# Performance work log

Hardware: AMD Instinct MI355X
Metric: run time of the kernel (lower is better)

The kernel has to match this reference:

```python
import jax, jax.numpy as jnp
import numpy as np

D_MODEL = 512
N_HEADS = 8
HEAD_DIM = D_MODEL // N_HEADS
TRUST_BIAS_SCALE = 0.1


def setup_inputs() -> dict:
    key = jax.random.key(0)
    ks = jax.random.split(key, 12)
    B, S, D, HD = 4, 2048, D_MODEL, HEAD_DIM
    s = 1.0 / np.sqrt(D)
    inp = {
        "x": jax.random.normal(ks[0], (B, S, D), dtype=jnp.float32),
        "trust_scores": jax.random.uniform(ks[1], (B, S), dtype=jnp.float32),
        # Linear weights stored as [in, out] (y = x @ W + b), matching torch math.
        "Wq": jax.random.normal(ks[2], (D, D), dtype=jnp.float32) * s,
        "bq": jnp.zeros((D,), dtype=jnp.float32),
        "Wk": jax.random.normal(ks[3], (D, D), dtype=jnp.float32) * s,
        "bk": jnp.zeros((D,), dtype=jnp.float32),
        "Wv": jax.random.normal(ks[4], (D, D), dtype=jnp.float32) * s,
        "bv": jnp.zeros((D,), dtype=jnp.float32),
        # trust_projection: nn.Linear(1, head_dim) -> weight vector [HD]
        "Wt": jax.random.normal(ks[5], (HD,), dtype=jnp.float32),
        "bt": jnp.zeros((HD,), dtype=jnp.float32),
        # trust_gate: nn.Linear(d_model + 1, d_model)
        "Wg": jax.random.normal(ks[6], (D + 1, D), dtype=jnp.float32) * s,
        "bg": jnp.zeros((D,), dtype=jnp.float32),
        "Wo": jax.random.normal(ks[7], (D, D), dtype=jnp.float32) * s,
        "bo": jnp.zeros((D,), dtype=jnp.float32),
    }
    return inp


def reference(x, trust_scores, Wq, bq, Wk, bk, Wv, bv, Wt, bt, Wg, bg, Wo, bo):
    B, S, D = x.shape
    H, HD = N_HEADS, HEAD_DIM

    # q/k/v projections -> [B, H, S, HD]
    q = (x @ Wq + bq).reshape(B, S, H, HD).transpose(0, 2, 1, 3)
    k = (x @ Wk + bk).reshape(B, S, H, HD).transpose(0, 2, 1, 3)
    v = (x @ Wv + bv).reshape(B, S, H, HD).transpose(0, 2, 1, 3)

    scores = jnp.einsum("bhqd,bhkd->bhqk", q, k) / jnp.sqrt(jnp.float32(HD))

    # trust bias: project scalar trust per turn into head_dim, outer-product affinity
    trust_proj = trust_scores[..., None] * Wt + bt            # [B, S, HD]
    trust_affinity = jax.nn.sigmoid(
        jnp.einsum("bqd,bkd->bqk", trust_proj, trust_proj))   # [B, S, S]
    scores = scores + TRUST_BIAS_SCALE * trust_affinity[:, None]  # broadcast heads

    attn = jax.nn.softmax(scores, axis=-1)                    # dropout is identity (eval)
    attended = jnp.einsum("bhqk,bhkd->bqhd", attn, v).reshape(B, S, D)

    # trust gating before output projection
    gate_in = jnp.concatenate([attended, trust_scores[..., None]], axis=-1)
    gate = jax.nn.sigmoid(gate_in @ Wg + bg)
    out = (attended * gate) @ Wo + bo
    return out, attn
```

## Files before the change

### kernel.cpp

```cpp
#include <hip/hip_runtime.h>
#include <math.h>

#define SEQ 2048
#define DM 512
#define NHH 8
#define NB 4
#define MR (NB*SEQ)
#define NBH (NB*NHH)

typedef __attribute__((ext_vector_type(8))) short bf16x8;
typedef __attribute__((ext_vector_type(4))) float f32x4;
#define MFMA __builtin_amdgcn_mfma_f32_16x16x32_bf16

#define OFF_XB   0ull
#define OFF_QB   8388608ull
#define OFF_KB   16777216ull
#define OFF_VB   25165824ull
#define OFF_ATTF 33554432ull
#define OFF_WQT  50331648ull
#define OFF_WKT  50855936ull
#define OFF_WVT  51380224ull
#define OFF_WGT  51904512ull
#define OFF_WOT  52428800ull
#define OFF_TS   52953088ull
#define OUT_ATTN 4194304ull

__device__ __forceinline__ unsigned short f2b(float f) {
  union { float f; unsigned u; } v; v.f = f;
  unsigned r = v.u + 0x7FFFu + ((v.u >> 16) & 1u);
  return (unsigned short)(r >> 16);
}
__device__ __forceinline__ float b2f(unsigned v16) {
  union { unsigned u; float f; } v; v.u = v16 << 16; return v.f;
}
__device__ __forceinline__ float sigm(float x) { return 1.0f / (1.0f + __expf(-x)); }

__global__ void k_trust_scalars(const float* __restrict__ Wt,
                                const float* __restrict__ bt,
                                float* __restrict__ ts) {
  int l = threadIdx.x;
  float w = Wt[l], b = bt[l];
  float a = w * w, bb = w * b, c = b * b;
  #pragma unroll
  for (int off = 32; off; off >>= 1) {
    a  += __shfl_down(a, off);
    bb += __shfl_down(bb, off);
    c  += __shfl_down(c, off);
  }
  if (l == 0) { ts[0] = a; ts[1] = bb; ts[2] = c; }
}

__global__ __launch_bounds__(256) void k_cvt_x(const float* __restrict__ x,
                                               unsigned short* __restrict__ xb) {
  const int i = (blockIdx.x * 256 + threadIdx.x) * 8;
  float4 a = *(const float4*)(x + i);
  float4 b = *(const float4*)(x + i + 4);
  uint4 o;
  o.x = (unsigned)f2b(a.x) | ((unsigned)f2b(a.y) << 16);
  o.y = (unsigned)f2b(a.z) | ((unsigned)f2b(a.w) << 16);
  o.z = (unsigned)f2b(b.x) | ((unsigned)f2b(b.y) << 16);
  o.w = (unsigned)f2b(b.z) | ((unsigned)f2b(b.w) << 16);
  *(uint4*)(xb + i) = o;
}

__global__ __launch_bounds__(256) void k_wtrans(const float* __restrict__ W,
                                                unsigned short* __restrict__ Wt) {
  __shared__ unsigned short tile[64][74];
  const int k0 = blockIdx.x * 64, n0 = blockIdx.y * 64, t = threadIdx.x;
  const int rr = t >> 4, c4 = (t & 15) * 4;
  #pragma unroll
  for (int rep = 0; rep < 4; rep++) {
    const int r = rr + rep * 16;
    float4 v = *(const float4*)(W + (size_t)(k0 + r) * 512 + n0 + c4);
    tile[c4][r] = f2b(v.x); tile[c4 + 1][r] = f2b(v.y);
    tile[c4 + 2][r] = f2b(v.z); tile[c4 + 3][r] = f2b(v.w);
  }
  __syncthreads();
  #pragma unroll
  for (int rep = 0; rep < 4; rep++) {
    const int n = rr + rep * 16;
    const unsigned short* p = &tile[n][c4];
    uint2 o;
    o.x = (unsigned)p[0] | ((unsigned)p[1] << 16);
    o.y = (unsigned)p[2] | ((unsigned)p[3] << 16);
    *(uint2*)(Wt + (size_t)(n0 + n) * 512 + k0 + c4) = o;
  }
}

__global__ __launch_bounds__(256) void k_vtrans(const unsigned short* __restrict__ Vb,
                                                unsigned short* __restrict__ Vt) {
  __shared__ unsigned short tile[64][74];
  const int s0 = blockIdx.x * 64;
  const int bh = blockIdx.y, b = bh >> 3, h = bh & 7;
  const int t = threadIdx.x, rr = t >> 4, c4 = (t & 15) * 4;
  #pragma unroll
  for (int rep = 0; rep < 4; rep++) {
    const int r = rr + rep * 16;
    uint2 v = *(const uint2*)(Vb + (size_t)(b * SEQ + s0 + r) * 512 + h * 64 + c4);
    tile[c4][r] = v.x & 0xffff; tile[c4 + 1][r] = v.x >> 16;
    tile[c4 + 2][r] = v.y & 0xffff; tile[c4 + 3][r] = v.y >> 16;
  }
  __syncthreads();
  #pragma unroll
  for (int rep = 0; rep < 4; rep++) {
    const int d = rr + rep * 16;
    const unsigned short* p = &tile[d][c4];
    uint2 o;
    o.x = (unsigned)p[0] | ((unsigned)p[1] << 16);
    o.y = (unsigned)p[2] | ((unsigned)p[3] << 16);
    *(uint2*)(Vt + (size_t)(bh * 64 + d) * SEQ + s0 + c4) = o;
  }
}

__global__ __launch_bounds__(256) void k_gemm(
    const unsigned short* __restrict__ A, const unsigned short* __restrict__ Bt,
    const float* __restrict__ bias, const float* __restrict__ wg512,
    const float* __restrict__ trust, const float* __restrict__ Afp,
    unsigned short* __restrict__ obf, float* __restrict__ ofp, int mode) {
  __shared__ unsigned short As[8][64][8];
  __shared__ unsigned short Bs[8][128][8];
  const int t = threadIdx.x;
  const int m0 = blockIdx.x * 64, n0 = blockIdx.y * 128;
  const int w = t >> 6, lane = t & 63, g = lane >> 4, ln = lane & 15;
  const int wm = w >> 1, wn = w & 1;

  f32x4 acc[2][4];
  #pragma unroll
  for (int i = 0; i < 2; i++)
    #pragma unroll
    for (int j = 0; j < 4; j++) acc[i][j] = (f32x4){0.f, 0.f, 0.f, 0.f};

  const int arow = t >> 2, apart = t & 3;
  const int brow = t >> 1, bhalf = t & 1;

  for (int k0 = 0; k0 < 512; k0 += 64) {
    __syncthreads();
    {
      const uint4* ga = (const uint4*)(A + (size_t)(m0 + arow) * 512 + k0 + apart * 16);
      uint4 u0 = ga[0], u1 = ga[1];
      *(uint4*)&As[apart * 2][arow][0]     = u0;
      *(uint4*)&As[apart * 2 + 1][arow][0] = u1;
      const uint4* gb = (const uint4*)(Bt + (size_t)(n0 + brow) * 512 + k0 + bhalf * 32);
      uint4 v0 = gb[0], v1 = gb[1], v2 = gb[2], v3 = gb[3];
      *(uint4*)&Bs[bhalf * 4][brow][0]     = v0;
      *(uint4*)&Bs[bhalf * 4 + 1][brow][0] = v1;
      *(uint4*)&Bs[bhalf * 4 + 2][brow][0] = v2;
      *(uint4*)&Bs[bhalf * 4 + 3][brow][0] = v3;
    }
    __syncthreads();
    #pragma unroll
    for (int ks = 0; ks < 2; ks++) {
      bf16x8 af[2], bfr[4];
      #pragma unroll
      for (int i = 0; i < 2; i++)
        af[i] = *(const bf16x8*)&As[ks * 4 + g][wm * 32 + i * 16 + ln][0];
      #pragma unroll
      for (int j = 0; j < 4; j++)
        bfr[j] = *(const bf16x8*)&Bs[ks * 4 + g][wn * 64 + j * 16 + ln][0];
      #pragma unroll
      for (int i = 0; i < 2; i++)
        #pragma unroll
        for (int j = 0; j < 4; j++)
          acc[i][j] = MFMA(af[i], bfr[j], acc[i][j], 0, 0, 0);
    }
  }

  #pragma unroll
  for (int j = 0; j < 4; j++) {
    const int n = n0 + wn * 64 + j * 16 + ln;
    const float bn = bias[n];
    const float wgn = (mode == 1) ? wg512[n] : 0.f;
    #pragma unroll
    for (int i = 0; i < 2; i++) {
      #pragma unroll
      for (int r = 0; r < 4; r++) {
        const int m = m0 + wm * 32 + i * 16 + g * 4 + r;
        const float v = acc[i][j][r] + bn;
        if (mode == 0) {
          obf[(size_t)m * 512 + n] = f2b(v);
        } else if (mode == 1) {
          const float gate = sigm(v + trust[m] * wgn);
          obf[(size_t)m * 512 + n] = f2b(Afp[(size_t)m * 512 + n] * gate);
        } else {
          ofp[(size_t)m * 512 + n] = v;
        }
      }
    }
  }
}

__global__ __launch_bounds__(512) void k_attn(
    const unsigned short* __restrict__ Qb, const unsigned short* __restrict__ Kb,
    const unsigned short* __restrict__ Vt, const float* __restrict__ trust,
    const float* __restrict__ ts, float* __restrict__ attn,
    float* __restrict__ attf, unsigned short* __restrict__ attb) {
  __shared__ unsigned short pb[32][2056];
  __shared__ float tks[2048];
  __shared__ float attS[32][68];
  __shared__ float Lsum[32];
  __shared__ float invLs[32];

  const int t = threadIdx.x;
  const int q0 = blockIdx.x * 32;
  const int bh = blockIdx.y, b = bh >> 3, h = bh & 7;
  const int w = t >> 6, lane = t & 63, g = lane >> 4, ln = lane & 15;

  *(float4*)(tks + t * 4) = *(const float4*)(trust + b * SEQ + t * 4);
  if (t < 32) Lsum[t] = 0.f;
  const float sa = ts[0], sb = ts[1], sc = ts[2];
  __syncthreads();

  const int qh = w & 1, kr = w >> 1;
  const unsigned short* qptr = Qb + (size_t)(b * SEQ + q0 + qh * 16 + ln) * 512 + h * 64;
  const bf16x8 qf0 = *(const bf16x8*)(qptr + g * 8);
  const bf16x8 qf1 = *(const bf16x8*)(qptr + 32 + g * 8);
  float tq[4];
  #pragma unroll
  for (int r = 0; r < 4; r++) tq[r] = tks[q0 + qh * 16 + g * 4 + r];
  float rs[4] = {0.f, 0.f, 0.f, 0.f};

  #pragma unroll 2
  for (int kt = 0; kt < 32; kt++) {
    const int k0 = kr * 512 + kt * 16;
    const unsigned short* kptr = Kb + (size_t)(b * SEQ + k0 + ln) * 512 + h * 64;
    const bf16x8 kf0 = *(const bf16x8*)(kptr + g * 8);
    const bf16x8 kf1 = *(const bf16x8*)(kptr + 32 + g * 8);
    f32x4 acc = (f32x4){0.f, 0.f, 0.f, 0.f};
    acc = MFMA(qf0, kf0, acc, 0, 0, 0);
    acc = MFMA(qf1, kf1, acc, 0, 0, 0);
    const float tkn = tks[k0 + ln];
    #pragma unroll
    for (int r = 0; r < 4; r++) {
      const float aff = sigm(sa * tq[r] * tkn + sb * (tq[r] + tkn) + sc);
      const float s = acc[r] * 0.125f + 0.1f * aff;
      const float p = __expf(s);
      rs[r] += p;
      pb[qh * 16 + g * 4 + r][k0 + ln] = f2b(p);
    }
  }
  #pragma unroll
  for (int r = 0; r < 4; r++) {
    float v = rs[r];
    v += __shfl_xor(v, 1); v += __shfl_xor(v, 2);
    v += __shfl_xor(v, 4); v += __shfl_xor(v, 8);
    if (ln == 0) atomicAdd(&Lsum[qh * 16 + g * 4 + r], v);
  }
  __syncthreads();
  if (t < 32) invLs[t] = 1.f / Lsum[t];
  __syncthreads();

  {
    const int row = t >> 4, c0 = (t & 15) * 4;
    const float il = invLs[row];
    float* dst = attn + ((size_t)bh * SEQ + q0 + row) * SEQ;
    #pragma unroll 4
    for (int it = 0; it < 32; it++) {
      const int c = it * 64 + c0;
      const uint2 v = *(const uint2*)&pb[row][c];
      float4 o;
      o.x = b2f(v.x & 0xffffu) * il; o.y = b2f(v.x >> 16) * il;
      o.z = b2f(v.y & 0xffffu) * il; o.w = b2f(v.y >> 16) * il;
      *(float4*)(dst + c) = o;
    }
  }

  {
    const int dt = w & 3, qh2 = w >> 2;
    f32x4 a0 = (f32x4){0.f, 0.f, 0.f, 0.f}, a1 = a0;
    const unsigned short* vrow = Vt + (size_t)(bh * 64 + dt * 16 + ln) * SEQ;
    const unsigned short* prow = &pb[qh2 * 16 + ln][0];
    #pragma unroll 4
    for (int kt = 0; kt < 32; kt++) {
      const bf16x8 v0 = *(const bf16x8*)(vrow + kt * 32 + g * 8);
      const bf16x8 p0 = *(const bf16x8*)(prow + kt * 32 + g * 8);
      a0 = MFMA(v0, p0, a0, 0, 0, 0);
      const bf16x8 v1 = *(const bf16x8*)(vrow + 1024 + kt * 32 + g * 8);
      const bf16x8 p1 = *(const bf16x8*)(prow + 1024 + kt * 32 + g * 8);
      a1 = MFMA(v1, p1, a1, 0, 0, 0);
    }
    const float il = invLs[qh2 * 16 + ln];
    #pragma unroll
    for (int r = 0; r < 4; r++)
      attS[qh2 * 16 + ln][dt * 16 + g * 4 + r] = (a0[r] + a1[r]) * il;
  }
  __syncthreads();
  {
    const int row = t >> 4, d0 = (t & 15) * 4;
    const size_t gbase = (size_t)(b * SEQ + q0 + row) * 512 + h * 64 + d0;
    const float4 v = *(const float4*)&attS[row][d0];
    *(float4*)(attf + gbase) = v;
    uint2 o;
    o.x = (unsigned)f2b(v.x) | ((unsigned)f2b(v.y) << 16);
    o.y = (unsigned)f2b(v.z) | ((unsigned)f2b(v.w) << 16);
    *(uint2*)(attb + gbase) = o;
  }
}

extern "C" void kernel_launch(void* const* d_in, const int* in_sizes, int n_in,
                              void* d_out, int out_size, void* d_ws, size_t ws_size,
                              hipStream_t stream) {
  const float* x     = (const float*)d_in[0];
  const float* trust = (const float*)d_in[1];
  const float* Wq = (const float*)d_in[2];  const float* bq = (const float*)d_in[3];
  const float* Wk = (const float*)d_in[4];  const float* bk = (const float*)d_in[5];
  const float* Wv = (const float*)d_in[6];  const float* bv = (const float*)d_in[7];
  const float* Wt = (const float*)d_in[8];  const float* bt = (const float*)d_in[9];
  const float* Wg = (const float*)d_in[10]; const float* bg = (const float*)d_in[11];
  const float* Wo = (const float*)d_in[12]; const float* bo = (const float*)d_in[13];

  float* out  = (float*)d_out;
  float* attn = out + OUT_ATTN;
  char* ws = (char*)d_ws;

  unsigned short* xb   = (unsigned short*)(ws + OFF_XB);
  unsigned short* Qb   = (unsigned short*)(ws + OFF_QB);
  unsigned short* Kb   = (unsigned short*)(ws + OFF_KB);
  unsigned short* Vb   = (unsigned short*)(ws + OFF_VB);
  unsigned short* Vtb  = (unsigned short*)(ws + OFF_XB);
  unsigned short* attb = (unsigned short*)(ws + OFF_VB);
  unsigned short* gatb = (unsigned short*)(ws + OFF_KB);
  float* attf = (float*)(ws + OFF_ATTF);
  unsigned short* Wqt = (unsigned short*)(ws + OFF_WQT);
  unsigned short* Wkt = (unsigned short*)(ws + OFF_WKT);
  unsigned short* Wvt = (unsigned short*)(ws + OFF_WVT);
  unsigned short* Wgt = (unsigned short*)(ws + OFF_WGT);
  unsigned short* Wot = (unsigned short*)(ws + OFF_WOT);
  float* tsp = (float*)(ws + OFF_TS);

  k_trust_scalars<<<1, 64, 0, stream>>>(Wt, bt, tsp);
  k_cvt_x<<<2048, 256, 0, stream>>>(x, xb);
  dim3 wg(8, 8);
  k_wtrans<<<wg, 256, 0, stream>>>(Wq, Wqt);
  k_wtrans<<<wg, 256, 0, stream>>>(Wk, Wkt);
  k_wtrans<<<wg, 256, 0, stream>>>(Wv, Wvt);
  k_wtrans<<<wg, 256, 0, stream>>>(Wg, Wgt);
  k_wtrans<<<wg, 256, 0, stream>>>(Wo, Wot);

  dim3 gg(128, 4);
  k_gemm<<<gg, 256, 0, stream>>>(xb, Wqt, bq, nullptr, nullptr, nullptr, Qb, nullptr, 0);
  k_gemm<<<gg, 256, 0, stream>>>(xb, Wkt, bk, nullptr, nullptr, nullptr, Kb, nullptr, 0);
  k_gemm<<<gg, 256, 0, stream>>>(xb, Wvt, bv, nullptr, nullptr, nullptr, Vb, nullptr, 0);

  k_vtrans<<<dim3(32, 32), 256, 0, stream>>>(Vb, Vtb);

  k_attn<<<dim3(64, 32), 512, 0, stream>>>(Qb, Kb, Vtb, trust, tsp, attn, attf, attb);

  k_gemm<<<gg, 256, 0, stream>>>(attb, Wgt, bg, Wg + 512 * 512, trust, attf,
                                 gatb, nullptr, 1);
  k_gemm<<<gg, 256, 0, stream>>>(gatb, Wot, bo, nullptr, nullptr, nullptr,
                                 nullptr, out, 2);
}
```

Before: 987.9 us.

## Fuse QKV projections, restructure attention into 16-row blocks with swizzled LDS

```diff
diff --git a/kernel.cpp b/kernel.cpp
--- a/kernel.cpp
+++ b/kernel.cpp
@@ -1,29 +1,23 @@
 #include <hip/hip_runtime.h>
-#include <math.h>
 
 #define SEQ 2048
-#define DM 512
-#define NHH 8
 #define NB 4
-#define MR (NB*SEQ)
-#define NBH (NB*NHH)
+#define NBH 32
 
 typedef __attribute__((ext_vector_type(8))) short bf16x8;
 typedef __attribute__((ext_vector_type(4))) float f32x4;
 #define MFMA __builtin_amdgcn_mfma_f32_16x16x32_bf16
 
-#define OFF_XB   0ull
+#define OFF_VT   0ull
 #define OFF_QB   8388608ull
 #define OFF_KB   16777216ull
 #define OFF_VB   25165824ull
 #define OFF_ATTF 33554432ull
 #define OFF_WQT  50331648ull
-#define OFF_WKT  50855936ull
-#define OFF_WVT  51380224ull
-#define OFF_WGT  51904512ull
-#define OFF_WOT  52428800ull
-#define OFF_TS   52953088ull
+#define OFF_BCAT 52953088ull
+#define OFF_TS   52959232ull
 #define OUT_ATTN 4194304ull
+#define MATSTR   (8192ull*512ull)
 
 __device__ __forceinline__ unsigned short f2b(float f) {
   union { float f; unsigned u; } v; v.f = f;
@@ -35,32 +29,24 @@
 }
 __device__ __forceinline__ float sigm(float x) { return 1.0f / (1.0f + __expf(-x)); }
 
-__global__ void k_trust_scalars(const float* __restrict__ Wt,
-                                const float* __restrict__ bt,
-                                float* __restrict__ ts) {
-  int l = threadIdx.x;
-  float w = Wt[l], b = bt[l];
-  float a = w * w, bb = w * b, c = b * b;
-  #pragma unroll
-  for (int off = 32; off; off >>= 1) {
-    a  += __shfl_down(a, off);
-    bb += __shfl_down(bb, off);
-    c  += __shfl_down(c, off);
-  }
-  if (l == 0) { ts[0] = a; ts[1] = bb; ts[2] = c; }
-}
-
-__global__ __launch_bounds__(256) void k_cvt_x(const float* __restrict__ x,
-                                               unsigned short* __restrict__ xb) {
-  const int i = (blockIdx.x * 256 + threadIdx.x) * 8;
-  float4 a = *(const float4*)(x + i);
-  float4 b = *(const float4*)(x + i + 4);
-  uint4 o;
-  o.x = (unsigned)f2b(a.x) | ((unsigned)f2b(a.y) << 16);
-  o.y = (unsigned)f2b(a.z) | ((unsigned)f2b(a.w) << 16);
-  o.z = (unsigned)f2b(b.x) | ((unsigned)f2b(b.y) << 16);
-  o.w = (unsigned)f2b(b.z) | ((unsigned)f2b(b.w) << 16);
-  *(uint4*)(xb + i) = o;
+__global__ __launch_bounds__(512) void k_prep(
+    const float* __restrict__ Wt, const float* __restrict__ bt,
+    const float* __restrict__ bq, const float* __restrict__ bk,
+    const float* __restrict__ bv, float* __restrict__ bcat,
+    float* __restrict__ ts) {
+  const int t = threadIdx.x;
+  if (t < 64) {
+    float w = Wt[t], b = bt[t];
+    float a = w * w, ab = w * b, c = b * b;
+    #pragma unroll
+    for (int off = 32; off; off >>= 1) {
+      a  += __shfl_down(a, off);
+      ab += __shfl_down(ab, off);
+      c  += __shfl_down(c, off);
+    }
+    if (t == 0) { ts[0] = a; ts[1] = ab; ts[2] = c; }
+  }
+  bcat[t] = bq[t]; bcat[512 + t] = bk[t]; bcat[1024 + t] = bv[t];
 }
 
 __global__ __launch_bounds__(256) void k_wtrans(const float* __restrict__ W,
@@ -113,16 +99,19 @@
 }
 
 __global__ __launch_bounds__(256) void k_gemm(
-    const unsigned short* __restrict__ A, const unsigned short* __restrict__ Bt,
-    const float* __restrict__ bias, const float* __restrict__ wg512,
-    const float* __restrict__ trust, const float* __restrict__ Afp,
-    unsigned short* __restrict__ obf, float* __restrict__ ofp, int mode) {
-  __shared__ unsigned short As[8][64][8];
-  __shared__ unsigned short Bs[8][128][8];
+    const float* __restrict__ Af, const unsigned short* __restrict__ Ab,
+    const unsigned short* __restrict__ Bt, const float* __restrict__ bcat,
+    const float* __restrict__ wg512, const float* __restrict__ trust,
+    const float* __restrict__ Afp, unsigned short* __restrict__ obf,
+    float* __restrict__ ofp, int mode) {
+  __shared__ union SU {
+    struct { unsigned short As[8][64][8]; unsigned short Bs[8][128][8]; } s;
+    float ct[64][66];
+  } u;
   const int t = threadIdx.x;
   const int m0 = blockIdx.x * 64, n0 = blockIdx.y * 128;
-  const int w = t >> 6, lane = t & 63, g = lane >> 4, ln = lane & 15;
-  const int wm = w >> 1, wn = w & 1;
+  const int w4 = t >> 6, lane = t & 63, g = lane >> 4, ln = lane & 15;
+  const int wm = w4 >> 1, wn = w4 & 1;
 
   f32x4 acc[2][4];
   #pragma unroll
@@ -130,22 +119,37 @@
     #pragma unroll
     for (int j = 0; j < 4; j++) acc[i][j] = (f32x4){0.f, 0.f, 0.f, 0.f};
 
-  const int arow = t >> 2, apart = t & 3;
-  const int brow = t >> 1, bhalf = t & 1;
-
+  const int am = t & 63, akk = t >> 6;
+  const int bn = t & 127, bk0 = t >> 7;
+
+  #pragma unroll 1
   for (int k0 = 0; k0 < 512; k0 += 64) {
     __syncthreads();
+    if (mode == 0) {
+      const float* ap = Af + (size_t)(m0 + am) * 512 + k0 + akk * 8;
+      float4 a0 = *(const float4*)ap,        a1 = *(const float4*)(ap + 4);
+      float4 a2 = *(const float4*)(ap + 32), a3 = *(const float4*)(ap + 36);
+      uint4 c0, c1;
+      c0.x = (unsigned)f2b(a0.x) | ((unsigned)f2b(a0.y) << 16);
+      c0.y = (unsigned)f2b(a0.z) | ((unsigned)f2b(a0.w) << 16);
+      c0.z = (unsigned)f2b(a1.x) | ((unsigned)f2b(a1.y) << 16);
+      c0.w = (unsigned)f2b(a1.z) | ((unsigned)f2b(a1.w) << 16);
+      c1.x = (unsigned)f2b(a2.x) | ((unsigned)f2b(a2.y) << 16);
+      c1.y = (unsigned)f2b(a2.z) | ((unsigned)f2b(a2.w) << 16);
+      c1.z = (unsigned)f2b(a3.x) | ((unsigned)f2b(a3.y) << 16);
+      c1.w = (unsigned)f2b(a3.z) | ((unsigned)f2b(a3.w) << 16);
+      *(uint4*)&u.s.As[akk][am][0]     = c0;
+      *(uint4*)&u.s.As[akk + 4][am][0] = c1;
+    } else {
+      const unsigned short* ap = Ab + (size_t)(m0 + am) * 512 + k0 + akk * 8;
+      *(uint4*)&u.s.As[akk][am][0]     = *(const uint4*)ap;
+      *(uint4*)&u.s.As[akk + 4][am][0] = *(const uint4*)(ap + 32);
+    }
     {
-      const uint4* ga = (const uint4*)(A + (size_t)(m0 + arow) * 512 + k0 + apart * 16);
-      uint4 u0 = ga[0], u1 = ga[1];
-      *(uint4*)&As[apart * 2][arow][0]     = u0;
-      *(uint4*)&As[apart * 2 + 1][arow][0] = u1;
-      const uint4* gb = (const uint4*)(Bt + (size_t)(n0 + brow) * 512 + k0 + bhalf * 32);
-      uint4 v0 = gb[0], v1 = gb[1], v2 = gb[2], v3 = gb[3];
-      *(uint4*)&Bs[bhalf * 4][brow][0]     = v0;
-      *(uint4*)&Bs[bhalf * 4 + 1][brow][0] = v1;
-      *(uint4*)&Bs[bhalf * 4 + 2][brow][0] = v2;
-      *(uint4*)&Bs[bhalf * 4 + 3][brow][0] = v3;
+      const unsigned short* bp = Bt + (size_t)(n0 + bn) * 512 + k0 + bk0 * 8;
+      #pragma unroll
+      for (int qq = 0; qq < 4; qq++)
+        *(uint4*)&u.s.Bs[bk0 + 2 * qq][bn][0] = *(const uint4*)(bp + qq * 16);
     }
     __syncthreads();
     #pragma unroll
@@ -153,10 +157,10 @@
       bf16x8 af[2], bfr[4];
       #pragma unroll
       for (int i = 0; i < 2; i++)
-        af[i] = *(const bf16x8*)&As[ks * 4 + g][wm * 32 + i * 16 + ln][0];
+        af[i] = *(const bf16x8*)&u.s.As[ks * 4 + g][wm * 32 + i * 16 + ln][0];
       #pragma unroll
       for (int j = 0; j < 4; j++)
-        bfr[j] = *(const bf16x8*)&Bs[ks * 4 + g][wn * 64 + j * 16 + ln][0];
+        bfr[j] = *(const bf16x8*)&u.s.Bs[ks * 4 + g][wn * 64 + j * 16 + ln][0];
       #pragma unroll
       for (int i = 0; i < 2; i++)
         #pragma unroll
@@ -165,25 +169,78 @@
     }
   }
 
-  #pragma unroll
-  for (int j = 0; j < 4; j++) {
-    const int n = n0 + wn * 64 + j * 16 + ln;
-    const float bn = bias[n];
-    const float wgn = (mode == 1) ? wg512[n] : 0.f;
-    #pragma unroll
-    for (int i = 0; i < 2; i++) {
-      #pragma unroll
-      for (int r = 0; r < 4; r++) {
-        const int m = m0 + wm * 32 + i * 16 + g * 4 + r;
-        const float v = acc[i][j][r] + bn;
-        if (mode == 0) {
-          obf[(size_t)m * 512 + n] = f2b(v);
-        } else if (mode == 1) {
-          const float gate = sigm(v + trust[m] * wgn);
-          obf[(size_t)m * 512 + n] = f2b(Afp[(size_t)m * 512 + n] * gate);
-        } else {
-          ofp[(size_t)m * 512 + n] = v;
-        }
+  float bj[4];
+  #pragma unroll
+  for (int j = 0; j < 4; j++) bj[j] = bcat[n0 + wn * 64 + j * 16 + ln];
+
+  #pragma unroll 1
+  for (int h = 0; h < 2; h++) {
+    __syncthreads();
+    if (wn == h) {
+      #pragma unroll
+      for (int i = 0; i < 2; i++)
+        #pragma unroll
+        for (int j = 0; j < 4; j++)
+          #pragma unroll
+          for (int r = 0; r < 4; r++)
+            u.ct[wm * 32 + i * 16 + g * 4 + r][j * 16 + ln] = acc[i][j][r] + bj[j];
+    }
+    __syncthreads();
+    {
+      const int row = t >> 2, c0 = (t & 3) << 4;
+      const int m = m0 + row;
+      float v[16];
+      *(float4*)(v)      = *(const float4*)&u.ct[row][c0];
+      *(float4*)(v + 4)  = *(const float4*)&u.ct[row][c0 + 4];
+      *(float4*)(v + 8)  = *(const float4*)&u.ct[row][c0 + 8];
+      *(float4*)(v + 12) = *(const float4*)&u.ct[row][c0 + 12];
+      if (mode == 0) {
+        const int ncg = n0 + h * 64 + c0;
+        const int mat = ncg >> 9, nc = ncg & 511;
+        unsigned short* op = obf + (size_t)mat * MATSTR + (size_t)m * 512 + nc;
+        uint4 o0, o1;
+        o0.x = (unsigned)f2b(v[0]) | ((unsigned)f2b(v[1]) << 16);
+        o0.y = (unsigned)f2b(v[2]) | ((unsigned)f2b(v[3]) << 16);
+        o0.z = (unsigned)f2b(v[4]) | ((unsigned)f2b(v[5]) << 16);
+        o0.w = (unsigned)f2b(v[6]) | ((unsigned)f2b(v[7]) << 16);
+        o1.x = (unsigned)f2b(v[8]) | ((unsigned)f2b(v[9]) << 16);
+        o1.y = (unsigned)f2b(v[10]) | ((unsigned)f2b(v[11]) << 16);
+        o1.z = (unsigned)f2b(v[12]) | ((unsigned)f2b(v[13]) << 16);
+        o1.w = (unsigned)f2b(v[14]) | ((unsigned)f2b(v[15]) << 16);
+        *(uint4*)op = o0; *(uint4*)(op + 8) = o1;
+      } else if (mode == 1) {
+        const int nc = n0 + h * 64 + c0;
+        const float tr = trust[m];
+        float wv[16], av[16];
+        *(float4*)(wv)      = *(const float4*)(wg512 + nc);
+        *(float4*)(wv + 4)  = *(const float4*)(wg512 + nc + 4);
+        *(float4*)(wv + 8)  = *(const float4*)(wg512 + nc + 8);
+        *(float4*)(wv + 12) = *(const float4*)(wg512 + nc + 12);
+        const float* app = Afp + (size_t)m * 512 + nc;
+        *(float4*)(av)      = *(const float4*)(app);
+        *(float4*)(av + 4)  = *(const float4*)(app + 4);
+        *(float4*)(av + 8)  = *(const float4*)(app + 8);
+        *(float4*)(av + 12) = *(const float4*)(app + 12);
+        #pragma unroll
+        for (int e = 0; e < 16; e++) v[e] = av[e] * sigm(v[e] + tr * wv[e]);
+        unsigned short* op = obf + (size_t)m * 512 + nc;
+        uint4 o0, o1;
+        o0.x = (unsigned)f2b(v[0]) | ((unsigned)f2b(v[1]) << 16);
+        o0.y = (unsigned)f2b(v[2]) | ((unsigned)f2b(v[3]) << 16);
+        o0.z = (unsigned)f2b(v[4]) | ((unsigned)f2b(v[5]) << 16);
+        o0.w = (unsigned)f2b(v[6]) | ((unsigned)f2b(v[7]) << 16);
+        o1.x = (unsigned)f2b(v[8]) | ((unsigned)f2b(v[9]) << 16);
+        o1.y = (unsigned)f2b(v[10]) | ((unsigned)f2b(v[11]) << 16);
+        o1.z = (unsigned)f2b(v[12]) | ((unsigned)f2b(v[13]) << 16);
+        o1.w = (unsigned)f2b(v[14]) | ((unsigned)f2b(v[15]) << 16);
+        *(uint4*)op = o0; *(uint4*)(op + 8) = o1;
+      } else {
+        const int nc = n0 + h * 64 + c0;
+        float* op = ofp + (size_t)m * 512 + nc;
+        *(float4*)(op)      = *(const float4*)(v);
+        *(float4*)(op + 4)  = *(const float4*)(v + 4);
+        *(float4*)(op + 8)  = *(const float4*)(v + 8);
+        *(float4*)(op + 12) = *(const float4*)(v + 12);
       }
     }
   }
@@ -194,105 +251,112 @@
     const unsigned short* __restrict__ Vt, const float* __restrict__ trust,
     const float* __restrict__ ts, float* __restrict__ attn,
     float* __restrict__ attf, unsigned short* __restrict__ attb) {
-  __shared__ unsigned short pb[32][2056];
+  __shared__ unsigned short pb[16 * 2048];
   __shared__ float tks[2048];
-  __shared__ float attS[32][68];
-  __shared__ float Lsum[32];
-  __shared__ float invLs[32];
+  __shared__ float attS[16][72];
+  __shared__ float Lsum[16];
+  __shared__ float invLs[16];
 
   const int t = threadIdx.x;
-  const int q0 = blockIdx.x * 32;
+  const int q0 = blockIdx.x * 16;
   const int bh = blockIdx.y, b = bh >> 3, h = bh & 7;
   const int w = t >> 6, lane = t & 63, g = lane >> 4, ln = lane & 15;
+  const int kslice = w * 256;
 
   *(float4*)(tks + t * 4) = *(const float4*)(trust + b * SEQ + t * 4);
-  if (t < 32) Lsum[t] = 0.f;
-  const float sa = ts[0], sb = ts[1], sc = ts[2];
-  __syncthreads();
-
-  const int qh = w & 1, kr = w >> 1;
-  const unsigned short* qptr = Qb + (size_t)(b * SEQ + q0 + qh * 16 + ln) * 512 + h * 64;
-  const bf16x8 qf0 = *(const bf16x8*)(qptr + g * 8);
-  const bf16x8 qf1 = *(const bf16x8*)(qptr + 32 + g * 8);
-  float tq[4];
-  #pragma unroll
-  for (int r = 0; r < 4; r++) tq[r] = tks[q0 + qh * 16 + g * 4 + r];
-  float rs[4] = {0.f, 0.f, 0.f, 0.f};
+  if (t < 16) Lsum[t] = 0.f;
+  for (int i = t; i < 16 * 72; i += 512) ((float*)attS)[i] = 0.f;
+  const float sa = ts[0], sbb = ts[1], scc = ts[2];
+  __syncthreads();
+
+  const unsigned short* qrow = Qb + ((size_t)(b * SEQ + q0 + ln)) * 512 + h * 64;
+  const bf16x8 qf0 = *(const bf16x8*)(qrow + g * 8);
+  const bf16x8 qf1 = *(const bf16x8*)(qrow + 32 + g * 8);
+  const float tq = tks[q0 + ln];
+  float rsum = 0.f;
+  const int swq = (ln & 7) << 4;
+  char* prowq = (char*)pb + ln * 4096;
 
   #pragma unroll 2
-  for (int kt = 0; kt < 32; kt++) {
-    const int k0 = kr * 512 + kt * 16;
-    const unsigned short* kptr = Kb + (size_t)(b * SEQ + k0 + ln) * 512 + h * 64;
-    const bf16x8 kf0 = *(const bf16x8*)(kptr + g * 8);
-    const bf16x8 kf1 = *(const bf16x8*)(kptr + 32 + g * 8);
+  for (int kt = 0; kt < 16; kt++) {
+    const int kb = kslice + kt * 16;
+    const unsigned short* krow = Kb + ((size_t)(b * SEQ + kb + ln)) * 512 + h * 64;
+    const bf16x8 kf0 = *(const bf16x8*)(krow + g * 8);
+    const bf16x8 kf1 = *(const bf16x8*)(krow + 32 + g * 8);
     f32x4 acc = (f32x4){0.f, 0.f, 0.f, 0.f};
-    acc = MFMA(qf0, kf0, acc, 0, 0, 0);
-    acc = MFMA(qf1, kf1, acc, 0, 0, 0);
-    const float tkn = tks[k0 + ln];
+    acc = MFMA(kf0, qf0, acc, 0, 0, 0);
+    acc = MFMA(kf1, qf1, acc, 0, 0, 0);
+    unsigned short po[4];
     #pragma unroll
     for (int r = 0; r < 4; r++) {
-      const float aff = sigm(sa * tq[r] * tkn + sb * (tq[r] + tkn) + sc);
-      const float s = acc[r] * 0.125f + 0.1f * aff;
-      const float p = __expf(s);
-      rs[r] += p;
-      pb[qh * 16 + g * 4 + r][k0 + ln] = f2b(p);
-    }
-  }
-  #pragma unroll
-  for (int r = 0; r < 4; r++) {
-    float v = rs[r];
-    v += __shfl_xor(v, 1); v += __shfl_xor(v, 2);
-    v += __shfl_xor(v, 4); v += __shfl_xor(v, 8);
-    if (ln == 0) atomicAdd(&Lsum[qh * 16 + g * 4 + r], v);
-  }
-  __syncthreads();
-  if (t < 32) invLs[t] = 1.f / Lsum[t];
+      const float tk = tks[kb + g * 4 + r];
+      const float y = 0.1f * sigm(sa * tq * tk + sbb * (tq + tk) + scc);
+      const float p = __expf(acc[r] * 0.125f) * (1.f + y + 0.5f * y * y);
+      rsum += p;
+      po[r] = f2b(p);
+    }
+    *(uint2*)(prowq + (((kb + g * 4) * 2) ^ swq)) = *(uint2*)po;
+  }
+  rsum += __shfl_xor(rsum, 16);
+  rsum += __shfl_xor(rsum, 32);
+  if (lane < 16) atomicAdd(&Lsum[ln], rsum);
+  __syncthreads();
+  if (t < 16) invLs[t] = 1.f / Lsum[t];
   __syncthreads();
 
   {
-    const int row = t >> 4, c0 = (t & 15) * 4;
+    const int row = t >> 5, lr = t & 31;
     const float il = invLs[row];
     float* dst = attn + ((size_t)bh * SEQ + q0 + row) * SEQ;
+    const char* src = (const char*)pb + row * 4096;
+    const int sw = (row & 7) << 4;
     #pragma unroll 4
-    for (int it = 0; it < 32; it++) {
-      const int c = it * 64 + c0;
-      const uint2 v = *(const uint2*)&pb[row][c];
+    for (int it = 0; it < 16; it++) {
+      const int colb = it * 256 + lr * 8;
+      const uint2 v = *(const uint2*)(src + (colb ^ sw));
       float4 o;
       o.x = b2f(v.x & 0xffffu) * il; o.y = b2f(v.x >> 16) * il;
       o.z = b2f(v.y & 0xffffu) * il; o.w = b2f(v.y >> 16) * il;
-      *(float4*)(dst + c) = o;
+      *(float4*)(dst + it * 128 + lr * 4) = o;
     }
   }
 
   {
-    const int dt = w & 3, qh2 = w >> 2;
-    f32x4 a0 = (f32x4){0.f, 0.f, 0.f, 0.f}, a1 = a0;
-    const unsigned short* vrow = Vt + (size_t)(bh * 64 + dt * 16 + ln) * SEQ;
-    const unsigned short* prow = &pb[qh2 * 16 + ln][0];
-    #pragma unroll 4
-    for (int kt = 0; kt < 32; kt++) {
-      const bf16x8 v0 = *(const bf16x8*)(vrow + kt * 32 + g * 8);
-      const bf16x8 p0 = *(const bf16x8*)(prow + kt * 32 + g * 8);
-      a0 = MFMA(v0, p0, a0, 0, 0, 0);
-      const bf16x8 v1 = *(const bf16x8*)(vrow + 1024 + kt * 32 + g * 8);
-      const bf16x8 p1 = *(const bf16x8*)(prow + 1024 + kt * 32 + g * 8);
-      a1 = MFMA(v1, p1, a1, 0, 0, 0);
-    }
-    const float il = invLs[qh2 * 16 + ln];
-    #pragma unroll
-    for (int r = 0; r < 4; r++)
-      attS[qh2 * 16 + ln][dt * 16 + g * 4 + r] = (a0[r] + a1[r]) * il;
-  }
-  __syncthreads();
-  {
+    f32x4 pacc[4];
+    #pragma unroll
+    for (int dt = 0; dt < 4; dt++) pacc[dt] = (f32x4){0.f, 0.f, 0.f, 0.f};
+    const char* prow = (const char*)pb + ln * 4096;
+    const int sw = (ln & 7) << 4;
+    #pragma unroll 2
+    for (int ks = 0; ks < 8; ks++) {
+      const int kb = kslice + ks * 32;
+      const bf16x8 pf = *(const bf16x8*)(prow + ((kb * 2 + g * 16) ^ sw));
+      #pragma unroll
+      for (int dt = 0; dt < 4; dt++) {
+        const bf16x8 vf =
+            *(const bf16x8*)(Vt + ((size_t)(bh * 64 + dt * 16 + ln)) * SEQ + kb + g * 8);
+        pacc[dt] = MFMA(vf, pf, pacc[dt], 0, 0, 0);
+      }
+    }
+    #pragma unroll
+    for (int dt = 0; dt < 4; dt++)
+      #pragma unroll
+      for (int r = 0; r < 4; r++)
+        atomicAdd(&attS[ln][dt * 16 + g * 4 + r], pacc[dt][r]);
+  }
+  __syncthreads();
+
+  if (t < 256) {
     const int row = t >> 4, d0 = (t & 15) * 4;
-    const size_t gbase = (size_t)(b * SEQ + q0 + row) * 512 + h * 64 + d0;
-    const float4 v = *(const float4*)&attS[row][d0];
-    *(float4*)(attf + gbase) = v;
+    const float il = invLs[row];
+    float4 v = *(const float4*)&attS[row][d0];
+    v.x *= il; v.y *= il; v.z *= il; v.w *= il;
+    const size_t gb = ((size_t)(b * SEQ + q0 + row)) * 512 + h * 64 + d0;
+    *(float4*)(attf + gb) = v;
     uint2 o;
     o.x = (unsigned)f2b(v.x) | ((unsigned)f2b(v.y) << 16);
     o.y = (unsigned)f2b(v.z) | ((unsigned)f2b(v.w) << 16);
-    *(uint2*)(attb + gbase) = o;
+    *(uint2*)(attb + gb) = o;
   }
 }
 
@@ -312,23 +376,22 @@
   float* attn = out + OUT_ATTN;
   char* ws = (char*)d_ws;
 
-  unsigned short* xb   = (unsigned short*)(ws + OFF_XB);
+  unsigned short* Vtb  = (unsigned short*)(ws + OFF_VT);
   unsigned short* Qb   = (unsigned short*)(ws + OFF_QB);
   unsigned short* Kb   = (unsigned short*)(ws + OFF_KB);
   unsigned short* Vb   = (unsigned short*)(ws + OFF_VB);
-  unsigned short* Vtb  = (unsigned short*)(ws + OFF_XB);
   unsigned short* attb = (unsigned short*)(ws + OFF_VB);
   unsigned short* gatb = (unsigned short*)(ws + OFF_KB);
   float* attf = (float*)(ws + OFF_ATTF);
   unsigned short* Wqt = (unsigned short*)(ws + OFF_WQT);
-  unsigned short* Wkt = (unsigned short*)(ws + OFF_WKT);
-  unsigned short* Wvt = (unsigned short*)(ws + OFF_WVT);
-  unsigned short* Wgt = (unsigned short*)(ws + OFF_WGT);
-  unsigned short* Wot = (unsigned short*)(ws + OFF_WOT);
-  float* tsp = (float*)(ws + OFF_TS);
-
-  k_trust_scalars<<<1, 64, 0, stream>>>(Wt, bt, tsp);
-  k_cvt_x<<<2048, 256, 0, stream>>>(x, xb);
+  unsigned short* Wkt = Wqt + 512 * 512;
+  unsigned short* Wvt = Wkt + 512 * 512;
+  unsigned short* Wgt = Wvt + 512 * 512;
+  unsigned short* Wot = Wgt + 512 * 512;
+  float* bcat = (float*)(ws + OFF_BCAT);
+  float* tsp  = (float*)(ws + OFF_TS);
+
+  k_prep<<<1, 512, 0, stream>>>(Wt, bt, bq, bk, bv, bcat, tsp);
   dim3 wg(8, 8);
   k_wtrans<<<wg, 256, 0, stream>>>(Wq, Wqt);
   k_wtrans<<<wg, 256, 0, stream>>>(Wk, Wkt);
@@ -336,17 +399,16 @@
   k_wtrans<<<wg, 256, 0, stream>>>(Wg, Wgt);
   k_wtrans<<<wg, 256, 0, stream>>>(Wo, Wot);
 
-  dim3 gg(128, 4);
-  k_gemm<<<gg, 256, 0, stream>>>(xb, Wqt, bq, nullptr, nullptr, nullptr, Qb, nullptr, 0);
-  k_gemm<<<gg, 256, 0, stream>>>(xb, Wkt, bk, nullptr, nullptr, nullptr, Kb, nullptr, 0);
-  k_gemm<<<gg, 256, 0, stream>>>(xb, Wvt, bv, nullptr, nullptr, nullptr, Vb, nullptr, 0);
+  k_gemm<<<dim3(128, 12), 256, 0, stream>>>(x, nullptr, Wqt, bcat, nullptr,
+                                            nullptr, nullptr, Qb, nullptr, 0);
 
   k_vtrans<<<dim3(32, 32), 256, 0, stream>>>(Vb, Vtb);
 
-  k_attn<<<dim3(64, 32), 512, 0, stream>>>(Qb, Kb, Vtb, trust, tsp, attn, attf, attb);
-
-  k_gemm<<<gg, 256, 0, stream>>>(attb, Wgt, bg, Wg + 512 * 512, trust, attf,
-                                 gatb, nullptr, 1);
-  k_gemm<<<gg, 256, 0, stream>>>(gatb, Wot, bo, nullptr, nullptr, nullptr,
-                                 nullptr, out, 2);
-}
+  k_attn<<<dim3(128, 32), 512, 0, stream>>>(Qb, Kb, Vtb, trust, tsp,
+                                            attn, attf, attb);
+
+  k_gemm<<<dim3(128, 4), 256, 0, stream>>>(nullptr, attb, Wgt, bg, Wg + 512 * 512,
+                                           trust, attf, gatb, nullptr, 1);
+  k_gemm<<<dim3(128, 4), 256, 0, stream>>>(nullptr, gatb, Wot, bo, nullptr,
+                                           nullptr, nullptr, nullptr, out, 2);
+}
```

Result: slower. 1.060 ms (+7.3%).
